# Performance work log

Hardware: AMD Instinct MI355X
Metric: run time of the kernel (lower is better)

The kernel has to match this reference:

```python
import jax, jax.numpy as jnp
import numpy as np

H_DIM = 256
N_HEADS = 8
HALF = H_DIM // 2

def _lin(x, W, b):
    # torch nn.Linear: y = x @ W.T + b
    y = x @ W.T
    return y + b if b is not None else y

def setup_inputs() -> dict:
    key = jax.random.key(0)
    ks = jax.random.split(key, 16)
    s = 0.02
    d = {
        'x': jax.random.normal(ks[0], (16, H_DIM, 32, 32), jnp.float32),
        'q1_w': jax.random.normal(ks[1], (HALF, HALF), jnp.float32) * s,
        'q1_b': jnp.zeros((HALF,), jnp.float32),
        'q2_w': jax.random.normal(ks[2], (HALF, HALF), jnp.float32) * s,
        'q2_b': jnp.zeros((HALF,), jnp.float32),
        'k1_w': jax.random.normal(ks[3], (HALF, HALF), jnp.float32) * s,
        'k1_b': jnp.zeros((HALF,), jnp.float32),
        'k2_w': jax.random.normal(ks[4], (HALF, HALF), jnp.float32) * s,
        'k2_b': jnp.zeros((HALF,), jnp.float32),
        'v1_w': jax.random.normal(ks[5], (HALF, HALF), jnp.float32) * s,
        'v1_b': jnp.zeros((HALF,), jnp.float32),
        'v2_w': jax.random.normal(ks[6], (HALF, HALF), jnp.float32) * s,
        'v2_b': jnp.zeros((HALF,), jnp.float32),
        'proj1_w': jax.random.normal(ks[7], (HALF, HALF), jnp.float32) * s,
        'proj1_b': jnp.zeros((HALF,), jnp.float32),
        'proj2_w': jax.random.normal(ks[8], (HALF, HALF), jnp.float32) * s,
        'proj2_b': jnp.zeros((HALF,), jnp.float32),
        'logit_scale': jnp.log(10.0 * jnp.ones((N_HEADS, 1, 1), jnp.float32)),
        'mlp_w1': jax.random.normal(ks[9], (128, 2), jnp.float32) * s,
        'mlp_b1': jnp.zeros((128,), jnp.float32),
        'mlp_w2': jax.random.normal(ks[10], (N_HEADS, 128), jnp.float32) * s,
    }
    return d

def _rel_pos_index(h, w):
    # static (numpy) relative position index, shape [N, N]
    ch, cw = np.meshgrid(np.arange(h), np.arange(w), indexing='ij')
    coords = np.stack([ch.reshape(-1), cw.reshape(-1)])  # [2, N]
    rel = coords[:, :, None] - coords[:, None, :]         # [2, N, N]
    rel = rel.transpose(1, 2, 0)
    rel[:, :, 0] += h - 1
    rel[:, :, 1] += w - 1
    return rel[:, :, 0] * (2 * w - 1) + rel[:, :, 1]

def _forward(x, q1_w, q1_b, q2_w, q2_b, k1_w, k1_b, k2_w, k2_b,
             v1_w, v1_b, v2_w, v2_b, proj1_w, proj1_b, proj2_w, proj2_b,
             logit_scale, mlp_w1, mlp_b1, mlp_w2):
    b, c, h, w = x.shape
    N = h * w
    nh = N_HEADS
    hd = c // nh
    x3 = jnp.transpose(x, (0, 2, 3, 1)).reshape(b, N, c)
    x0, x1 = x3[..., :c // 2], x3[..., c // 2:]

    def qkv(W0, b0, W1, b1):
        t = jnp.concatenate([x0 + _lin(x0, W0, b0), x1 + _lin(x1, W1, b1)], axis=-1)
        return t.reshape(b, N, nh, hd).transpose(0, 2, 1, 3)  # [b, nh, N, hd]

    q = qkv(q1_w, q1_b, q2_w, q2_b)
    k = qkv(k1_w, k1_b, k2_w, k2_b)
    v = qkv(v1_w, v1_b, v2_w, v2_b)

    eps = 1e-12
    qn = q / jnp.maximum(jnp.linalg.norm(q, axis=-1, keepdims=True), eps)
    kn = k / jnp.maximum(jnp.linalg.norm(k, axis=-1, keepdims=True), eps)
    attn = jnp.einsum('bhnd,bhmd->bhnm', qn, kn)  # cosine similarity
    scale = jnp.exp(jnp.minimum(logit_scale, jnp.log(1.0 / 0.01)))  # [nh,1,1]
    attn = attn * scale[None]

    # continuous relative-position bias (CPB) table via small MLP
    rch = jnp.arange(-(h - 1), h, dtype=jnp.float32) / (h - 1 + 1e-8)
    rcw = jnp.arange(-(w - 1), w, dtype=jnp.float32) / (w - 1 + 1e-8)
    gh, gw = jnp.meshgrid(rch, rcw, indexing='ij')
    tab = jnp.stack([gh, gw], axis=-1) * 3.2               # [2h-1, 2w-1, 2]
    tab = jnp.sign(tab) * (1.0 - jnp.exp(-jnp.abs(tab)))
    tab = jax.nn.relu(_lin(tab, mlp_w1, mlp_b1))
    tab = _lin(tab, mlp_w2, None).reshape(-1, nh)          # [(2h-1)(2w-1), nh]

    idx = jnp.asarray(_rel_pos_index(h, w))                # [N, N]
    bias = tab[idx.reshape(-1)].reshape(N, N, nh).transpose(2, 0, 1)
    bias = 16.0 * jax.nn.sigmoid(bias)
    attn = attn + bias[None]

    attn = jax.nn.softmax(attn, axis=-1)
    out = jnp.einsum('bhnm,bhmd->bhnd', attn, v).transpose(0, 2, 1, 3).reshape(b, N, c)
    o0, o1 = out[..., :c // 2], out[..., c // 2:]
    out = jnp.concatenate([_lin(o0, proj1_w, proj1_b), _lin(o1, proj2_w, proj2_b)], axis=-1)
    return out.reshape(b, h, w, c).transpose(0, 3, 1, 2)

def reference(x, q1_w, q1_b, q2_w, q2_b, k1_w, k1_b, k2_w, k2_b,
              v1_w, v1_b, v2_w, v2_b, proj1_w, proj1_b, proj2_w, proj2_b,
              logit_scale, mlp_w1, mlp_b1, mlp_w2):
    return _forward(x, q1_w, q1_b, q2_w, q2_b, k1_w, k1_b, k2_w, k2_b,
                    v1_w, v1_b, v2_w, v2_b, proj1_w, proj1_b, proj2_w, proj2_b,
                    logit_scale, mlp_w1, mlp_b1, mlp_w2)
```

## Files before the change

kernel.cpp:

```cpp
#include <hip/hip_runtime.h>
#include <cmath>


typedef _Float16 half_t;
typedef __attribute__((ext_vector_type(4))) _Float16 half4;
typedef __attribute__((ext_vector_type(8))) _Float16 half8;
typedef __attribute__((ext_vector_type(4))) float float4v;

static __device__ __forceinline__ float4v mfma16(half8 a, half8 b, float4v c) {
  return __builtin_amdgcn_mfma_f32_16x16x32_f16(a, b, c, 0, 0, 0);
}

struct PtrArr8 { const float* p[8]; };

__global__ __launch_bounds__(256) void prep_w(PtrArr8 wsrc, PtrArr8 bsrc,
                                              half_t* __restrict__ wf,
                                              float* __restrict__ bws) {
  int y = blockIdx.y;
  const float* src = nullptr;
  const float* bs = nullptr;
#pragma unroll
  for (int i = 0; i < 8; i++)
    if (i == y) { src = wsrc.p[i]; bs = bsrc.p[i]; }
  int i0 = (blockIdx.x * 256 + threadIdx.x) * 4;
  float4 w = *(const float4*)(src + i0);
  int j = i0 >> 7, k = i0 & 127;
  float id0 = 0.f, id1 = 0.f, id2 = 0.f, id3 = 0.f;
  if (y < 6) {
    if (j == k)     id0 = 1.0f;
    if (j == k + 1) id1 = 1.0f;
    if (j == k + 2) id2 = 1.0f;
    if (j == k + 3) id3 = 1.0f;
  }
  half4 h;
  h[0] = (half_t)(w.x + id0);
  h[1] = (half_t)(w.y + id1);
  h[2] = (half_t)(w.z + id2);
  h[3] = (half_t)(w.w + id3);
  *(half4*)(wf + y * 16384 + i0) = h;
  if (blockIdx.x == 0 && threadIdx.x < 128)
    bws[y * 128 + threadIdx.x] = bs[threadIdx.x];
}

__global__ __launch_bounds__(256) void bias_mlp(const float* __restrict__ w1,
                                                const float* __restrict__ b1,
                                                const float* __restrict__ w2,
                                                const float* __restrict__ ls,
                                                float* __restrict__ tabh2) {
  __shared__ float sw1[256];
  __shared__ float sb1[128];
  __shared__ float sw2[1024];
  int t = threadIdx.x;
  sw1[t] = w1[t];
  if (t < 128) sb1[t] = b1[t];
  for (int i = t; i < 1024; i += 256) sw2[i] = w2[i];
  __syncthreads();
  int p = blockIdx.x * 256 + t;
  if (p >= 3969) return;
  int ph = p / 63, pw = p % 63;
  float t0 = (float)(ph - 31) * (3.2f / 31.0f);
  float t1 = (float)(pw - 31) * (3.2f / 31.0f);
  t0 = copysignf(1.0f - __expf(-fabsf(t0)), t0);
  t1 = copysignf(1.0f - __expf(-fabsf(t1)), t1);
  float acc[8];
#pragma unroll
  for (int hh = 0; hh < 8; hh++) acc[hh] = 0.0f;
  for (int j = 0; j < 128; j++) {
    float hj = fmaxf(0.0f, t0 * sw1[2 * j] + t1 * sw1[2 * j + 1] + sb1[j]);
#pragma unroll
    for (int hh = 0; hh < 8; hh++) acc[hh] += hj * sw2[hh * 128 + j];
  }
  const float L2E = 1.44269504f;
#pragma unroll
  for (int hh = 0; hh < 8; hh++) {
    float scale = __expf(fminf(ls[hh], 4.6051702f));
    float c14 = 14.0f - (scale + 16.0f) * L2E;
    float bias = 16.0f / (1.0f + __expf(-acc[hh]));
    tabh2[hh * 3969 + p] = bias * L2E + c14;
  }
}

__global__ __launch_bounds__(256) void qkv_mfma(
    const float* __restrict__ x, const half_t* __restrict__ wf,
    const float* __restrict__ lscale, const float* __restrict__ bws,
    half_t* __restrict__ qf, half_t* __restrict__ kf,
    half_t* __restrict__ vf) {
  __shared__ half_t wb[128 * 136];
  __shared__ half_t tbuf[128 * 68];
  int t = threadIdx.x;
  int lane = t & 63, wv = t >> 6, l = lane & 15, quad = lane >> 4;
  int hf = blockIdx.y;
  int m0 = blockIdx.x * 64;
  int b = m0 >> 10, n0 = m0 & 1023;

  half8 afr[4];
  {
    const float* xb = x + (size_t)b * 256 * 1024 + n0 + wv * 16 + l;
#pragma unroll
    for (int ks = 0; ks < 4; ks++) {
      int kbase = hf * 128 + ks * 32 + quad * 8;
      half8 a;
#pragma unroll
      for (int j = 0; j < 8; j++)
        a[j] = (half_t)xb[(size_t)(kbase + j) * 1024];
      afr[ks] = a;
    }
  }

  for (int op = 0; op < 3; op++) {
    int combo = op * 2 + hf;
    __syncthreads();
    {
      const half_t* wg = wf + combo * 16384;
#pragma unroll
      for (int i = 0; i < 8; i++) {
        int flat = (t + 256 * i) * 8;
        int row = flat >> 7, col = flat & 127;
        *(half8*)(wb + row * 136 + col) = *(const half8*)(wg + flat);
      }
    }
    __syncthreads();

    float4v acc[8];
#pragma unroll
    for (int ng = 0; ng < 8; ng++) {
      float4v c = {0.f, 0.f, 0.f, 0.f};
#pragma unroll
      for (int ks = 0; ks < 4; ks++) {
        half8 bfrag =
            *(const half8*)(wb + (ng * 16 + l) * 136 + ks * 32 + quad * 8);
        c = mfma16(afr[ks], bfrag, c);
      }
      acc[ng] = c;
    }
#pragma unroll
    for (int ng = 0; ng < 8; ng++) {
      float bb = bws[combo * 128 + ng * 16 + l];
#pragma unroll
      for (int r2 = 0; r2 < 4; r2++) acc[ng][r2] += bb;
    }
    if (op < 2) {
#pragma unroll
      for (int hg = 0; hg < 4; hg++) {
        float sc = 1.0f;
        if (op == 0)
          sc = __expf(fminf(lscale[hf * 4 + hg], 4.6051702f)) * 1.44269504f;
#pragma unroll
        for (int r2 = 0; r2 < 4; r2++) {
          float ss = acc[2 * hg][r2] * acc[2 * hg][r2] +
                     acc[2 * hg + 1][r2] * acc[2 * hg + 1][r2];
          ss += __shfl_xor(ss, 1, 64);
          ss += __shfl_xor(ss, 2, 64);
          ss += __shfl_xor(ss, 4, 64);
          ss += __shfl_xor(ss, 8, 64);
          float rn = sc / fmaxf(sqrtf(ss), 1e-12f);
          acc[2 * hg][r2] *= rn;
          acc[2 * hg + 1][r2] *= rn;
        }
      }
#pragma unroll
      for (int ng = 0; ng < 8; ng++)
#pragma unroll
        for (int r2 = 0; r2 < 4; r2++)
          tbuf[(wv * 16 + quad * 4 + r2) * 132 + ng * 16 + l] =
              (half_t)acc[ng][r2];
      __syncthreads();
      half_t* dst = (op == 0) ? qf : kf;
#pragma unroll
      for (int i = 0; i < 4; i++) {
        int idx = t + 256 * i;
        int row = idx >> 4, colc = (idx & 15) * 8;
        half8 vv = *(const half8*)(tbuf + row * 132 + colc);
        int head = hf * 4 + (colc >> 5), d = colc & 31;
        *(half8*)(dst + (((size_t)b * 8 + head) * 1024 + n0 + row) * 32 + d) =
            vv;
      }
    } else {
#pragma unroll
      for (int ng = 0; ng < 8; ng++) {
        int col = ng * 16 + l;
        half4 hv;
#pragma unroll
        for (int r2 = 0; r2 < 4; r2++) hv[r2] = (half_t)acc[ng][r2];
        *(half4*)(tbuf + col * 68 + wv * 16 + quad * 4) = hv;
      }
      __syncthreads();
#pragma unroll
      for (int i = 0; i < 16; i++) {
        int idx = t + 256 * i;
        int col = idx >> 5, rp = idx & 31;
        unsigned int val = *(const unsigned int*)(tbuf + col * 68 + rp * 2);
        int head = hf * 4 + (col >> 5);
        int d = col & 31;
        *(unsigned int*)((char*)vf +
                         (((((size_t)b * 8 + head) * 32 + d) * 1024) + n0 +
                          rp * 2) * 2) = val;
      }
    }
  }
}

__global__ __launch_bounds__(512) void attn_mfma(
    const half_t* __restrict__ qf, const half_t* __restrict__ kf,
    const half_t* __restrict__ vf, const float* __restrict__ tabh2,
    half_t* __restrict__ ao) {
  __shared__ float sb2[47 * 63];
  __shared__ half_t pa[8 * 16 * 80];

  int t = threadIdx.x;
  int lane = t & 63, wv = t >> 6, l = lane & 15, quad = lane >> 4;
  int qh = blockIdx.x, h = blockIdx.y, b = blockIdx.z;
  size_t bh = (size_t)b * 8 + h;
  const half_t* kbase = kf + bh * 1024 * 32;
  const half_t* vbase = vf + bh * 32 * 1024;

  for (int i = t; i < 2961; i += 512)
    sb2[i] = tabh2[h * 3969 + qh * 1008 + i];

  int row0 = qh * 512 + wv * 64;
  half8 qfr[4];
#pragma unroll
  for (int s = 0; s < 4; s++)
    qfr[s] =
        *(const half8*)(qf + (bh * 1024 + row0 + s * 16 + l) * 32 + quad * 8);

  float4v o0[4], o1[4];
  float run_l[4];
#pragma unroll
  for (int s = 0; s < 4; s++) {
    o0[s] = (float4v){0.f, 0.f, 0.f, 0.f};
    o1[s] = (float4v){0.f, 0.f, 0.f, 0.f};
    run_l[s] = 0.0f;
  }
  half_t* paw = pa + wv * 16 * 80;
  __syncthreads();

#pragma unroll 2
  for (int kt = 0; kt < 16; kt++) {
    half8 kfr[4], v0fr[2], v1fr[2];
#pragma unroll
    for (int nt = 0; nt < 4; nt++)
      kfr[nt] =
          *(const half8*)(kbase + (kt * 64 + nt * 16 + l) * 32 + quad * 8);
#pragma unroll
    for (int ks = 0; ks < 2; ks++) {
      v0fr[ks] = *(const half8*)(vbase + l * 1024 + kt * 64 + ks * 32 +
                                 quad * 8);
      v1fr[ks] = *(const half8*)(vbase + (16 + l) * 1024 + kt * 64 + ks * 32 +
                                 quad * 8);
    }
#pragma unroll
    for (int s = 0; s < 4; s++) {
      int ihl = 2 * wv + (s >> 1);
      float4v sres[4];
#pragma unroll
      for (int nt = 0; nt < 4; nt++) {
        int base = (ihl - 2 * kt - (nt >> 1) + 31) * 63 + (s & 1) * 16 + l +
                   31 - (nt & 1) * 16 - quad * 4;
        float4v c;
        c[0] = sb2[base];
        c[1] = sb2[base - 1];
        c[2] = sb2[base - 2];
        c[3] = sb2[base - 3];
        sres[nt] = mfma16(kfr[nt], qfr[s], c);
      }
#pragma unroll
      for (int nt = 0; nt < 4; nt++) {
        half4 ph;
#pragma unroll
        for (int r2 = 0; r2 < 4; r2++) {
          float p = exp2f(sres[nt][r2]);
          run_l[s] += p;
          ph[r2] = (half_t)p;
        }
        *(half4*)(paw + l * 80 + nt * 16 + quad * 4) = ph;
      }
#pragma unroll
      for (int ks = 0; ks < 2; ks++) {
        half8 pfr = *(const half8*)(paw + l * 80 + ks * 32 + quad * 8);
        o0[s] = mfma16(pfr, v0fr[ks], o0[s]);
        o1[s] = mfma16(pfr, v1fr[ks], o1[s]);
      }
    }
  }

#pragma unroll
  for (int s = 0; s < 4; s++) {
    float rl = run_l[s];
    rl += __shfl_xor(rl, 16, 64);
    rl += __shfl_xor(rl, 32, 64);
    float rli = 1.0f / rl;
#pragma unroll
    for (int r2 = 0; r2 < 4; r2++) {
      float linv = __shfl(rli, 20 * quad + r2, 64);
      size_t rowaddr =
          ((size_t)b * 1024 + row0 + s * 16 + quad * 4 + r2) * 256 + h * 32;
      ao[rowaddr + l] = (half_t)(o0[s][r2] * linv);
      ao[rowaddr + 16 + l] = (half_t)(o1[s][r2] * linv);
    }
  }
}

__global__ __launch_bounds__(256) void proj_mfma(
    const half_t* __restrict__ ao, const half_t* __restrict__ wp,
    const float* __restrict__ bws, float* __restrict__ out) {
  __shared__ half_t wb[128 * 136];
  __shared__ float yt[128 * 68];
  int t = threadIdx.x;
  int lane = t & 63, wv = t >> 6, l = lane & 15, quad = lane >> 4;
  int hf = blockIdx.y;
  int m0 = blockIdx.x * 64;
  int b = m0 >> 10, n0 = m0 & 1023;

  {
    const half_t* wg = wp + hf * 16384;
#pragma unroll
    for (int i = 0; i < 8; i++) {
      int flat = (t + 256 * i) * 8;
      int row = flat >> 7, col = flat & 127;
      *(half8*)(wb + row * 136 + col) = *(const half8*)(wg + flat);
    }
  }

  half8 afr[4];
  const half_t* ab =
      ao + ((size_t)m0 + wv * 16 + l) * 256 + hf * 128 + quad * 8;
#pragma unroll
  for (int ks = 0; ks < 4; ks++) afr[ks] = *(const half8*)(ab + ks * 32);
  __syncthreads();

#pragma unroll
  for (int ng = 0; ng < 8; ng++) {
    float4v c = {0.f, 0.f, 0.f, 0.f};
#pragma unroll
    for (int ks = 0; ks < 4; ks++)
      c = mfma16(afr[ks],
                 *(const half8*)(wb + (ng * 16 + l) * 136 + ks * 32 +
                                 quad * 8),
                 c);
    float bb = bws[(6 + hf) * 128 + ng * 16 + l];
#pragma unroll
    for (int r2 = 0; r2 < 4; r2++) c[r2] += bb;
    *(float4v*)(yt + (ng * 16 + l) * 68 + wv * 16 + quad * 4) = c;
  }
  __syncthreads();
#pragma unroll
  for (int i = 0; i < 8; i++) {
    int idx = t + 256 * i;
    int col = idx >> 4, rg = idx & 15;
    float4v vv = *(const float4v*)(yt + col * 68 + rg * 4);
    *(float4v*)(out + ((size_t)b * 256 + hf * 128 + col) * 1024 + n0 +
                rg * 4) = vv;
  }
}

extern "C" void kernel_launch(void* const* d_in, const int* in_sizes, int n_in,
                              void* d_out, int out_size, void* d_ws,
                              size_t ws_size, hipStream_t stream) {
  (void)in_sizes; (void)n_in; (void)out_size; (void)ws_size;
  const float* x = (const float*)d_in[0];

  half_t* ws = (half_t*)d_ws;
  half_t* qfp = ws;
  half_t* kfp = ws + 4194304;
  half_t* vfp = ws + 8388608;
  half_t* aop = ws + 12582912;
  half_t* wfp = ws + 16777216;
  float* tabh2 = (float*)((char*)d_ws + 33816576);
  float* bws = (float*)((char*)d_ws + 33943584);

  PtrArr8 wsrc, bsrc;
  const int widx[8] = {1, 3, 5, 7, 9, 11, 13, 15};
  for (int i = 0; i < 8; i++) {
    wsrc.p[i] = (const float*)d_in[widx[i]];
    bsrc.p[i] = (const float*)d_in[widx[i] + 1];
  }

  prep_w<<<dim3(16, 8), 256, 0, stream>>>(wsrc, bsrc, wfp, bws);
  bias_mlp<<<16, 256, 0, stream>>>((const float*)d_in[18],
                                   (const float*)d_in[19],
                                   (const float*)d_in[20],
                                   (const float*)d_in[17], tabh2);
  qkv_mfma<<<dim3(256, 2), 256, 0, stream>>>(x, wfp, (const float*)d_in[17],
                                             bws, qfp, kfp, vfp);
  attn_mfma<<<dim3(2, 8, 16), 512, 0, stream>>>(qfp, kfp, vfp, tabh2, aop);
  proj_mfma<<<dim3(256, 2), 256, 0, stream>>>(aop, wfp + 6 * 16384, bws,
                                              (float*)d_out);
}
```

Baseline: 194.7 us.

## Fuse weight conversion into GEMM kernels and shrink attention blocks

Drops the separate prep_w launch and has the qkv and proj kernels read fp32 weights and biases directly, converting them to half and adding the identity residual while staging into shared memory. This removes one kernel launch and a workspace round trip, but every block now repeats the conversion work. The attention kernel also moves from 512-thread blocks covering 512 query rows to 256-thread blocks covering 128 rows, with each wave handling 32 rows instead of 64. That quadruples the grid and cuts shared-memory use per block, at the cost of reloading K and V more times.

```diff
diff --git a/kernel.cpp b/kernel.cpp
--- a/kernel.cpp
+++ b/kernel.cpp
@@ -12,35 +12,6 @@
 }
 
 struct PtrArr8 { const float* p[8]; };
-
-__global__ __launch_bounds__(256) void prep_w(PtrArr8 wsrc, PtrArr8 bsrc,
-                                              half_t* __restrict__ wf,
-                                              float* __restrict__ bws) {
-  int y = blockIdx.y;
-  const float* src = nullptr;
-  const float* bs = nullptr;
-#pragma unroll
-  for (int i = 0; i < 8; i++)
-    if (i == y) { src = wsrc.p[i]; bs = bsrc.p[i]; }
-  int i0 = (blockIdx.x * 256 + threadIdx.x) * 4;
-  float4 w = *(const float4*)(src + i0);
-  int j = i0 >> 7, k = i0 & 127;
-  float id0 = 0.f, id1 = 0.f, id2 = 0.f, id3 = 0.f;
-  if (y < 6) {
-    if (j == k)     id0 = 1.0f;
-    if (j == k + 1) id1 = 1.0f;
-    if (j == k + 2) id2 = 1.0f;
-    if (j == k + 3) id3 = 1.0f;
-  }
-  half4 h;
-  h[0] = (half_t)(w.x + id0);
-  h[1] = (half_t)(w.y + id1);
-  h[2] = (half_t)(w.z + id2);
-  h[3] = (half_t)(w.w + id3);
-  *(half4*)(wf + y * 16384 + i0) = h;
-  if (blockIdx.x == 0 && threadIdx.x < 128)
-    bws[y * 128 + threadIdx.x] = bs[threadIdx.x];
-}
 
 __global__ __launch_bounds__(256) void bias_mlp(const float* __restrict__ w1,
                                                 const float* __restrict__ b1,
@@ -81,10 +52,9 @@
 }
 
 __global__ __launch_bounds__(256) void qkv_mfma(
-    const float* __restrict__ x, const half_t* __restrict__ wf,
-    const float* __restrict__ lscale, const float* __restrict__ bws,
-    half_t* __restrict__ qf, half_t* __restrict__ kf,
-    half_t* __restrict__ vf) {
+    const float* __restrict__ x, PtrArr8 wsrc, PtrArr8 bsrc,
+    const float* __restrict__ lscale, half_t* __restrict__ qf,
+    half_t* __restrict__ kf, half_t* __restrict__ vf) {
   __shared__ half_t wb[128 * 136];
   __shared__ half_t tbuf[128 * 68];
   int t = threadIdx.x;
@@ -109,15 +79,23 @@
 
   for (int op = 0; op < 3; op++) {
     int combo = op * 2 + hf;
+    const float* wg = nullptr;
+    const float* bg = nullptr;
+#pragma unroll
+    for (int i = 0; i < 6; i++)
+      if (i == combo) { wg = wsrc.p[i]; bg = bsrc.p[i]; }
     __syncthreads();
-    {
-      const half_t* wg = wf + combo * 16384;
-#pragma unroll
-      for (int i = 0; i < 8; i++) {
-        int flat = (t + 256 * i) * 8;
-        int row = flat >> 7, col = flat & 127;
-        *(half8*)(wb + row * 136 + col) = *(const half8*)(wg + flat);
-      }
+#pragma unroll
+    for (int i = 0; i < 16; i++) {
+      int flat = (t + 256 * i) * 4;
+      int row = flat >> 7, col = flat & 127;
+      float4 w = *(const float4*)(wg + flat);
+      half4 h;
+      h[0] = (half_t)(w.x + (col == row ? 1.0f : 0.0f));
+      h[1] = (half_t)(w.y + (col + 1 == row ? 1.0f : 0.0f));
+      h[2] = (half_t)(w.z + (col + 2 == row ? 1.0f : 0.0f));
+      h[3] = (half_t)(w.w + (col + 3 == row ? 1.0f : 0.0f));
+      *(half4*)(wb + row * 136 + col) = h;
     }
     __syncthreads();
 
@@ -135,7 +113,7 @@
     }
 #pragma unroll
     for (int ng = 0; ng < 8; ng++) {
-      float bb = bws[combo * 128 + ng * 16 + l];
+      float bb = bg[ng * 16 + l];
 #pragma unroll
       for (int r2 = 0; r2 < 4; r2++) acc[ng][r2] += bb;
     }
@@ -200,34 +178,34 @@
   }
 }
 
-__global__ __launch_bounds__(512) void attn_mfma(
+__global__ __launch_bounds__(256) void attn_mfma(
     const half_t* __restrict__ qf, const half_t* __restrict__ kf,
     const half_t* __restrict__ vf, const float* __restrict__ tabh2,
     half_t* __restrict__ ao) {
-  __shared__ float sb2[47 * 63];
-  __shared__ half_t pa[8 * 16 * 80];
+  __shared__ float sb2[35 * 63];
+  __shared__ half_t pa[4 * 16 * 80];
 
   int t = threadIdx.x;
   int lane = t & 63, wv = t >> 6, l = lane & 15, quad = lane >> 4;
-  int qh = blockIdx.x, h = blockIdx.y, b = blockIdx.z;
+  int qo = blockIdx.x, h = blockIdx.y, b = blockIdx.z;
   size_t bh = (size_t)b * 8 + h;
   const half_t* kbase = kf + bh * 1024 * 32;
   const half_t* vbase = vf + bh * 32 * 1024;
 
-  for (int i = t; i < 2961; i += 512)
-    sb2[i] = tabh2[h * 3969 + qh * 1008 + i];
-
-  int row0 = qh * 512 + wv * 64;
-  half8 qfr[4];
-#pragma unroll
-  for (int s = 0; s < 4; s++)
+  for (int i = t; i < 2205; i += 256)
+    sb2[i] = tabh2[h * 3969 + qo * 252 + i];
+
+  int row0 = qo * 128 + wv * 32;
+  half8 qfr[2];
+#pragma unroll
+  for (int s = 0; s < 2; s++)
     qfr[s] =
         *(const half8*)(qf + (bh * 1024 + row0 + s * 16 + l) * 32 + quad * 8);
 
-  float4v o0[4], o1[4];
-  float run_l[4];
-#pragma unroll
-  for (int s = 0; s < 4; s++) {
+  float4v o0[2], o1[2];
+  float run_l[2];
+#pragma unroll
+  for (int s = 0; s < 2; s++) {
     o0[s] = (float4v){0.f, 0.f, 0.f, 0.f};
     o1[s] = (float4v){0.f, 0.f, 0.f, 0.f};
     run_l[s] = 0.0f;
@@ -250,13 +228,12 @@
                                  quad * 8);
     }
 #pragma unroll
-    for (int s = 0; s < 4; s++) {
-      int ihl = 2 * wv + (s >> 1);
+    for (int s = 0; s < 2; s++) {
       float4v sres[4];
 #pragma unroll
       for (int nt = 0; nt < 4; nt++) {
-        int base = (ihl - 2 * kt - (nt >> 1) + 31) * 63 + (s & 1) * 16 + l +
-                   31 - (nt & 1) * 16 - quad * 4;
+        int base = (wv - 2 * kt - (nt >> 1) + 31) * 63 + s * 16 + l + 31 -
+                   (nt & 1) * 16 - quad * 4;
         float4v c;
         c[0] = sb2[base];
         c[1] = sb2[base - 1];
@@ -285,7 +262,7 @@
   }
 
 #pragma unroll
-  for (int s = 0; s < 4; s++) {
+  for (int s = 0; s < 2; s++) {
     float rl = run_l[s];
     rl += __shfl_xor(rl, 16, 64);
     rl += __shfl_xor(rl, 32, 64);
@@ -302,8 +279,8 @@
 }
 
 __global__ __launch_bounds__(256) void proj_mfma(
-    const half_t* __restrict__ ao, const half_t* __restrict__ wp,
-    const float* __restrict__ bws, float* __restrict__ out) {
+    const half_t* __restrict__ ao, PtrArr8 wsrc, PtrArr8 bsrc,
+    float* __restrict__ out) {
   __shared__ half_t wb[128 * 136];
   __shared__ float yt[128 * 68];
   int t = threadIdx.x;
@@ -312,14 +289,19 @@
   int m0 = blockIdx.x * 64;
   int b = m0 >> 10, n0 = m0 & 1023;
 
-  {
-    const half_t* wg = wp + hf * 16384;
-#pragma unroll
-    for (int i = 0; i < 8; i++) {
-      int flat = (t + 256 * i) * 8;
-      int row = flat >> 7, col = flat & 127;
-      *(half8*)(wb + row * 136 + col) = *(const half8*)(wg + flat);
-    }
+  const float* wg = hf ? wsrc.p[7] : wsrc.p[6];
+  const float* bg = hf ? bsrc.p[7] : bsrc.p[6];
+#pragma unroll
+  for (int i = 0; i < 16; i++) {
+    int flat = (t + 256 * i) * 4;
+    int row = flat >> 7, col = flat & 127;
+    float4 w = *(const float4*)(wg + flat);
+    half4 h;
+    h[0] = (half_t)w.x;
+    h[1] = (half_t)w.y;
+    h[2] = (half_t)w.z;
+    h[3] = (half_t)w.w;
+    *(half4*)(wb + row * 136 + col) = h;
   }
 
   half8 afr[4];
@@ -338,7 +320,7 @@
                  *(const half8*)(wb + (ng * 16 + l) * 136 + ks * 32 +
                                  quad * 8),
                  c);
-    float bb = bws[(6 + hf) * 128 + ng * 16 + l];
+    float bb = bg[ng * 16 + l];
 #pragma unroll
     for (int r2 = 0; r2 < 4; r2++) c[r2] += bb;
     *(float4v*)(yt + (ng * 16 + l) * 68 + wv * 16 + quad * 4) = c;
@@ -365,9 +347,7 @@
   half_t* kfp = ws + 4194304;
   half_t* vfp = ws + 8388608;
   half_t* aop = ws + 12582912;
-  half_t* wfp = ws + 16777216;
   float* tabh2 = (float*)((char*)d_ws + 33816576);
-  float* bws = (float*)((char*)d_ws + 33943584);
 
   PtrArr8 wsrc, bsrc;
   const int widx[8] = {1, 3, 5, 7, 9, 11, 13, 15};
@@ -376,14 +356,13 @@
     bsrc.p[i] = (const float*)d_in[widx[i] + 1];
   }
 
-  prep_w<<<dim3(16, 8), 256, 0, stream>>>(wsrc, bsrc, wfp, bws);
   bias_mlp<<<16, 256, 0, stream>>>((const float*)d_in[18],
                                    (const float*)d_in[19],
                                    (const float*)d_in[20],
                                    (const float*)d_in[17], tabh2);
-  qkv_mfma<<<dim3(256, 2), 256, 0, stream>>>(x, wfp, (const float*)d_in[17],
-                                             bws, qfp, kfp, vfp);
-  attn_mfma<<<dim3(2, 8, 16), 512, 0, stream>>>(qfp, kfp, vfp, tabh2, aop);
-  proj_mfma<<<dim3(256, 2), 256, 0, stream>>>(aop, wfp + 6 * 16384, bws,
-                                              (float*)d_out);
-}
+  qkv_mfma<<<dim3(256, 2), 256, 0, stream>>>(x, wsrc, bsrc,
+                                             (const float*)d_in[17], qfp, kfp,
+                                             vfp);
+  attn_mfma<<<dim3(8, 8, 16), 256, 0, stream>>>(qfp, kfp, vfp, tabh2, aop);
+  proj_mfma<<<dim3(256, 2), 256, 0, stream>>>(aop, wsrc, bsrc, (float*)d_out);
+}
```

New measurement: 226.2 us. 16.2% more time.
